# Optimization experiments

Hardware: AMD Instinct MI355X
Metric: run time of the kernel (lower is better)

Reference implementation:

```python
import jax, jax.numpy as jnp
import numpy as np

B, C, H, W = 1, 512, 64, 64
HEADS, DH = 8, 64
DI = HEADS * DH          # 512 = heads * dim_head
SW = 8                   # sliding window size
CB = 16                  # compress block size
SB = 2                   # selection block size
NSEL = 2                 # num selected blocks
N = H * W                # 4096 tokens
NCB = N // CB            # 256 compress blocks
NFB = N // SB            # 2048 fine (selection) blocks
NEG = jnp.finfo(jnp.float32).min


def setup_inputs() -> dict:
    key = jax.random.key(0)
    ks = jax.random.split(key, 24)
    rn = lambda k, shape, s=0.03: jax.random.normal(k, shape, jnp.float32) * s
    return dict(
        x=jax.random.normal(ks[0], (B, C, H, W), jnp.float32),
        w_in=rn(ks[1], (C, C)), b_in=jnp.zeros((C,), jnp.float32),
        g_norm=jnp.ones((C,), jnp.float32),
        wq=rn(ks[2], (DI, C)), wk=rn(ks[3], (DI, C)), wv=rn(ks[4], (DI, C)),
        k_pos=rn(ks[5], (HEADS, CB, DH), 0.02), v_pos=rn(ks[6], (HEADS, CB, DH), 0.02),
        mem_k=rn(ks[7], (HEADS, 1, DH), 0.02), mem_v=rn(ks[8], (HEADS, 1, DH), 0.02),
        kc_w1=rn(ks[9], (CB * DH, CB * DH)), kc_b1=jnp.zeros((CB * DH,), jnp.float32),
        kc_w2=rn(ks[10], (DH, CB * DH)), kc_b2=jnp.zeros((DH,), jnp.float32),
        vc_w1=rn(ks[11], (CB * DH, CB * DH)), vc_b1=jnp.zeros((CB * DH,), jnp.float32),
        vc_w2=rn(ks[12], (DH, CB * DH)), vc_b2=jnp.zeros((DH,), jnp.float32),
        w_strat=rn(ks[13], (3 * HEADS, C)), b_strat=jnp.zeros((3 * HEADS,), jnp.float32),
        w_comb=rn(ks[14], (C, DI)),
        w_out=rn(ks[15], (C, C)), b_out=jnp.zeros((C,), jnp.float32),
    )


def _rope(x):
    # rotary-embedding-torch default: theta=10000, interleaved pairs
    d = x.shape[-1]
    inv = 1.0 / (10000.0 ** (jnp.arange(0, d, 2, dtype=jnp.float32) / d))
    ang = jnp.arange(x.shape[-2], dtype=jnp.float32)[:, None] * inv  # (n, d/2)
    cos = jnp.repeat(jnp.cos(ang), 2, axis=-1)
    sin = jnp.repeat(jnp.sin(ang), 2, axis=-1)
    xp = x.reshape(x.shape[:-1] + (d // 2, 2))
    xr = jnp.stack((-xp[..., 1], xp[..., 0]), axis=-1).reshape(x.shape)
    return x * cos + xr * sin


def reference(x, w_in, b_in, g_norm, wq, wk, wv, k_pos, v_pos, mem_k, mem_v,
              kc_w1, kc_b1, kc_w2, kc_b2, vc_w1, vc_b1, vc_w2, vc_b2,
              w_strat, b_strat, w_comb, w_out, b_out):
    scale = DH ** -0.5
    # proj_in (1x1 conv) then flatten to sequence (b, n, c); residual uses this
    xs = jnp.einsum('bchw,oc->bohw', x, w_in) + b_in[None, :, None, None]
    seq = xs.reshape(B, C, N).transpose(0, 2, 1)
    # RMSNorm
    h = seq * jax.lax.rsqrt(jnp.mean(seq * seq, -1, keepdims=True) + 1e-6) * g_norm
    # qkv -> (b, heads, n, d)
    q = (h @ wq.T).reshape(B, N, HEADS, DH).transpose(0, 2, 1, 3)
    k = (h @ wk.T).reshape(B, N, HEADS, DH).transpose(0, 2, 1, 3)
    v = (h @ wv.T).reshape(B, N, HEADS, DH).transpose(0, 2, 1, 3)

    # ---- 1. compressed attention (block compression MLP + mem kv) ----
    kin = (k + jnp.tile(k_pos, (1, NCB, 1))[None]).reshape(B, HEADS, NCB, CB * DH)
    vin = (v + jnp.tile(v_pos, (1, NCB, 1))[None]).reshape(B, HEADS, NCB, CB * DH)
    ck = jax.nn.relu(kin @ kc_w1.T + kc_b1) @ kc_w2.T + kc_b2   # (b,h,NCB,d)
    cv = jax.nn.relu(vin @ vc_w1.T + vc_b1) @ vc_w2.T + vc_b2
    ck = jnp.concatenate([jnp.broadcast_to(mem_k[None], (B, HEADS, 1, DH)), ck], axis=2)
    cv = jnp.concatenate([jnp.broadcast_to(mem_v[None], (B, HEADS, 1, DH)), cv], axis=2)
    ck_seq = jnp.concatenate([jnp.array([-1]), (jnp.arange(NCB) + 1) * CB - 1])
    cmask = ck_seq[None, :] < jnp.arange(N)[:, None]             # (N, NCB+1), True=attend
    csim = jnp.einsum('bhid,bhjd->bhij', q, ck) * scale
    csim = jnp.where(cmask[None, None], csim, NEG)
    compressed_out = jnp.einsum('bhij,bhjd->bhid', jax.nn.softmax(csim, axis=-1), cv)

    # rotary positions for fine + sliding branches
    rq, rk = _rope(q), _rope(k)

    # ---- 2. fine selection attention ----
    # importance at fine-block granularity; since SB divides CB, each fine block
    # maps to exactly one compress block (equivalent to repeat->mask->mean in torch)
    imp = csim[..., 1:]                                          # drop mem kv logits
    fb_of = jnp.arange(NFB) // (CB // SB)
    imp_fine = imp[..., fb_of]                                   # (b,h,N,NFB)
    blk_causal = jnp.arange(NFB)[None, :] < (jnp.arange(N) // SB)[:, None]
    imp_fine = jnp.where(blk_causal[None, None], imp_fine, -jnp.inf)
    logits = jnp.concatenate([jnp.full((B, HEADS, N, 1), -1e3, jnp.float32), imp_fine], axis=-1)
    probs = jax.nn.softmax(logits, axis=-1)[..., 1:]             # (b,h,N,NFB)
    sel_val, sel_idx = jax.lax.top_k(probs, NSEL)                # (b,h,N,NSEL)
    diag_idx = jnp.broadcast_to((jnp.arange(N) // SB)[None, None, :, None], (B, HEADS, N, 1))
    sel_idx = jnp.concatenate([sel_idx, diag_idx], axis=-1)      # append own (diagonal) block
    fmask_sel = jnp.repeat((sel_val > 1e-10)[..., None], SB, axis=-1)   # (b,h,N,NSEL,SB)
    diag_mask = jnp.arange(SB)[None, :] <= (jnp.arange(N) % SB)[:, None]  # within-block causal
    diag_mask = jnp.broadcast_to(diag_mask[None, None, :, None, :], (B, HEADS, N, 1, SB))
    fmask = jnp.concatenate([fmask_sel, diag_mask], axis=-2).reshape(B, HEADS, N, (NSEL + 1) * SB)
    fk_blk = rk.reshape(B, HEADS, NFB, SB, DH)
    fv_blk = v.reshape(B, HEADS, NFB, SB, DH)
    idx = sel_idx.reshape(B, HEADS, N * (NSEL + 1))[..., None, None]
    fk = jnp.take_along_axis(fk_blk, idx, axis=2).reshape(B, HEADS, N, (NSEL + 1) * SB, DH)
    fv = jnp.take_along_axis(fv_blk, idx, axis=2).reshape(B, HEADS, N, (NSEL + 1) * SB, DH)
    fsim = jnp.einsum('bhid,bhijd->bhij', rq, fk) * scale
    fsim = jnp.where(fmask, fsim, NEG)
    fine_out = jnp.einsum('bhij,bhijd->bhid', jax.nn.softmax(fsim, axis=-1), fv)

    # ---- 3. sliding window attention (causal, exact window: 0 <= i-j <= SW) ----
    kp = jnp.pad(rk, ((0, 0), (0, 0), (SW, 0), (0, 0)))
    vp = jnp.pad(v, ((0, 0), (0, 0), (SW, 0), (0, 0)))
    widx = jnp.arange(N)[:, None] + jnp.arange(SW + 1)[None, :]  # indices into padded seq
    kw = kp[:, :, widx]                                          # (b,h,N,SW+1,d)
    vw = vp[:, :, widx]
    wvalid = (jnp.arange(N)[:, None] - SW + jnp.arange(SW + 1)[None, :]) >= 0
    ssim = jnp.einsum('bhid,bhijd->bhij', rq, kw) * scale
    ssim = jnp.where(wvalid[None, None], ssim, NEG)
    slide_out = jnp.einsum('bhij,bhijd->bhid', jax.nn.softmax(ssim, axis=-1), vw)

    # ---- combine the three strategies with learned sigmoid gates ----
    gates = jax.nn.sigmoid(h @ w_strat.T + b_strat).reshape(B, N, HEADS, 3).transpose(0, 2, 1, 3)
    out = gates[..., 0:1] * compressed_out + gates[..., 1:2] * fine_out + gates[..., 2:3] * slide_out
    out = out.transpose(0, 2, 1, 3).reshape(B, N, DI) @ w_comb.T  # merge heads + combine
    out2d = out.transpose(0, 2, 1).reshape(B, C, H, W)
    return jnp.einsum('bchw,oc->bohw', out2d, w_out) + b_out[None, :, None, None] + xs
```

## Files before the change

### kernel.cpp

```cpp
#include <hip/hip_runtime.h>
#include <hip/hip_bf16.h>
#include <math.h>

typedef __attribute__((ext_vector_type(8))) short s8v;
typedef __attribute__((ext_vector_type(8))) _Float16 h8v;
typedef __attribute__((ext_vector_type(4))) float f4v;
typedef __hip_bfloat16 bf16;

#define NEGF (-3.40282346638528859812e+38f)
#define QSMEM 20480
#define BSMEM 20480

enum { EPI_F32 = 0, EPI_BIAS, EPI_BRELU_BF16, EPI_BF16, EPI_FINAL };

__device__ __forceinline__ float wred_sum(float v) {
#pragma unroll
  for (int m = 1; m < 64; m <<= 1) v += __shfl_xor(v, m, 64);
  return v;
}

template <int EPI>
__device__ __forceinline__ void bgemm_body(char* smem, int bx, int by, int bz,
    const bf16* __restrict__ A, const bf16* __restrict__ B, void* __restrict__ C,
    int K, int ldC, long sA, long sB, long sC,
    const float* __restrict__ bias, const void* __restrict__ aux) {
  short (*Ahs)[2560] = (short(*)[2560])smem;
  short (*Bhs)[2560] = (short(*)[2560])(smem + 2 * 2560 * 2);
  const short* ah = (const short*)A + (long)bz * sA;
  const short* bh = (const short*)B + (long)bz * sB;
  int tid = threadIdx.x;
  int wv_ = tid >> 6, lane = tid & 63;
  int lrow = tid >> 2, lcol = (tid & 3) << 3;
  int lidx = lrow * 40 + lcol;
  long abase = (long)(bx * 64 + lrow) * K + lcol;
  long bbase = (long)(by * 64 + lrow) * K + lcol;
  int frow = lane & 15, fk = (lane >> 4) << 3;
  int aoff = (wv_ * 16 + frow) * 40 + fk;
  f4v acc[4] = {};
  {
    s8v avh = *(const s8v*)&ah[abase];
    s8v bvh = *(const s8v*)&bh[bbase];
    *(s8v*)&Ahs[0][lidx] = avh;
    *(s8v*)&Bhs[0][lidx] = bvh;
  }
  __syncthreads();
  int nit = K >> 5, buf = 0;
  s8v rAa, rAb, rBa, rBb;
  if (nit > 1) {
    rAa = *(const s8v*)&ah[abase + 32];
    rAb = *(const s8v*)&bh[bbase + 32];
  }
#define B_DSMFMA                                                       \
  {                                                                    \
    s8v afh = *(const s8v*)&Ahs[buf][aoff];                            \
    _Pragma("unroll") for (int nt = 0; nt < 4; nt++) {                 \
      s8v bfh = *(const s8v*)&Bhs[buf][(nt * 16 + frow) * 40 + fk];    \
      acc[nt] = __builtin_amdgcn_mfma_f32_16x16x32_bf16(afh, bfh, acc[nt], 0, 0, 0); \
    }                                                                  \
  }
  for (int it = 0; it < nit; it += 2) {
    if (it + 2 < nit) {
      long ko = (long)(it + 2) << 5;
      rBa = *(const s8v*)&ah[abase + ko];
      rBb = *(const s8v*)&bh[bbase + ko];
    }
    B_DSMFMA
    if (it + 1 < nit) {
      *(s8v*)&Ahs[buf ^ 1][lidx] = rAa;
      *(s8v*)&Bhs[buf ^ 1][lidx] = rAb;
      __syncthreads();
      buf ^= 1;
      if (it + 3 < nit) {
        long ko = (long)(it + 3) << 5;
        rAa = *(const s8v*)&ah[abase + ko];
        rAb = *(const s8v*)&bh[bbase + ko];
      }
      B_DSMFMA
      if (it + 2 < nit) {
        *(s8v*)&Ahs[buf ^ 1][lidx] = rBa;
        *(s8v*)&Bhs[buf ^ 1][lidx] = rBb;
        __syncthreads();
        buf ^= 1;
      }
    }
  }
#undef B_DSMFMA
  int rb = bx * 64 + wv_ * 16 + ((lane >> 4) << 2);
#pragma unroll
  for (int nt = 0; nt < 4; nt++) {
    int gn = by * 64 + nt * 16 + (lane & 15);
#pragma unroll
    for (int rg = 0; rg < 4; rg++) {
      int gm = rb + rg;
      float v = acc[nt][rg];
      long ci = (long)bz * sC + (long)gm * ldC + gn;
      if (EPI == EPI_F32) ((float*)C)[ci] = v;
      else if (EPI == EPI_BIAS) ((float*)C)[ci] = v + bias[gn];
      else if (EPI == EPI_BRELU_BF16) ((bf16*)C)[ci] = __float2bfloat16(fmaxf(v + bias[gn], 0.f));
      else if (EPI == EPI_BF16) ((bf16*)C)[ci] = __float2bfloat16(v);
      else if (EPI == EPI_FINAL)
        ((float*)C)[ci] = v + bias[gm] + ((const float*)aux)[(long)gn * 512 + gm];
    }
  }
}


#define HX_DECL                                                     \
  short* L = (short*)smem;                                          \
  const int MS = 64 * 40;                                           \
  int tid = threadIdx.x;                                            \
  int wv = tid >> 6, lane = tid & 63;                               \
  int lrow = tid >> 2, lcol = (tid & 3) << 3;                       \
  int frow = lane & 15, fk = (lane >> 4) << 3;                      \
  int aoff = (wv * 16 + frow) * 40 + fk;                            \
  int soff = lrow * 40 + lcol;                                      \
  f4v acc0[4] = {}, accx[4] = {}, acc2[4] = {};

#define HX_STAGE0                                                   \
  {                                                                 \
    *(h8v*)&L[0 * MS + soff] = *(const h8v*)&Ah[abase];             \
    *(h8v*)&L[1 * MS + soff] = *(const h8v*)&Al[abase];             \
    *(h8v*)&L[2 * MS + soff] = *(const h8v*)&Bh[bbase];             \
    *(h8v*)&L[3 * MS + soff] = *(const h8v*)&Bl[bbase];             \
  }                                                                 \
  __syncthreads();

#define HX_DSMFMA                                                   \
  {                                                                 \
    h8v ah = *(const h8v*)&L[aoff];                                 \
    h8v al = *(const h8v*)&L[MS + aoff];                            \
    _Pragma("unroll") for (int nt = 0; nt < 4; nt++) {              \
      int bo = 2 * MS + (nt * 16 + frow) * 40 + fk;                 \
      h8v bh = *(const h8v*)&L[bo];                                 \
      h8v bl = *(const h8v*)&L[bo + MS];                            \
      acc0[nt] = __builtin_amdgcn_mfma_f32_16x16x32_f16(ah, bh, acc0[nt], 0, 0, 0); \
      accx[nt] = __builtin_amdgcn_mfma_f32_16x16x32_f16(ah, bl, accx[nt], 0, 0, 0); \
      accx[nt] = __builtin_amdgcn_mfma_f32_16x16x32_f16(al, bh, accx[nt], 0, 0, 0); \
      acc2[nt] = __builtin_amdgcn_mfma_f32_16x16x32_f16(al, bl, acc2[nt], 0, 0, 0); \
    }                                                               \
  }

#define HX_LOOP(NIT)                                                \
  h8v rAa, rAb, rAc, rAd, rBa, rBb, rBc, rBd;                       \
  if ((NIT) > 1) {                                                  \
    rAa = *(const h8v*)&Ah[abase + 32];                             \
    rAb = *(const h8v*)&Al[abase + 32];                             \
    rAc = *(const h8v*)&Bh[bbase + 32];                             \
    rAd = *(const h8v*)&Bl[bbase + 32];                             \
  }                                                                 \
  for (int it = 0; it < (NIT); it += 2) {                           \
    if (it + 2 < (NIT)) {                                           \
      long ko = (long)(it + 2) << 5;                                \
      rBa = *(const h8v*)&Ah[abase + ko];                           \
      rBb = *(const h8v*)&Al[abase + ko];                           \
      rBc = *(const h8v*)&Bh[bbase + ko];                           \
      rBd = *(const h8v*)&Bl[bbase + ko];                           \
    }                                                               \
    HX_DSMFMA                                                       \
    if (it + 1 < (NIT)) {                                           \
      __syncthreads();                                              \
      *(h8v*)&L[soff] = rAa;                                        \
      *(h8v*)&L[MS + soff] = rAb;                                   \
      *(h8v*)&L[2 * MS + soff] = rAc;                               \
      *(h8v*)&L[3 * MS + soff] = rAd;                               \
      __syncthreads();                                              \
      if (it + 3 < (NIT)) {                                         \
        long ko = (long)(it + 3) << 5;                              \
        rAa = *(const h8v*)&Ah[abase + ko];                         \
        rAb = *(const h8v*)&Al[abase + ko];                         \
        rAc = *(const h8v*)&Bh[bbase + ko];                         \
        rAd = *(const h8v*)&Bl[bbase + ko];                         \
      }                                                             \
      HX_DSMFMA                                                     \
      if (it + 2 < (NIT)) {                                         \
        __syncthreads();                                            \
        *(h8v*)&L[soff] = rBa;                                      \
        *(h8v*)&L[MS + soff] = rBb;                                 \
        *(h8v*)&L[2 * MS + soff] = rBc;                             \
        *(h8v*)&L[3 * MS + soff] = rBd;                             \
      __syncthreads();                                              \
      }                                                             \
    }                                                               \
  }

#define HX_COMBINE(nt, rg) \
  (acc0[nt][rg] + (accx[nt][rg] + acc2[nt][rg] * (1.f / 4096.f)) * (1.f / 4096.f))

__device__ __forceinline__ void qk_f16_body(char* smem, int bx, int by,
    const _Float16* __restrict__ Ah, const _Float16* __restrict__ Al,
    const _Float16* __restrict__ Bh, const _Float16* __restrict__ Bl,
    _Float16* __restrict__ qhh, _Float16* __restrict__ qhl,
    _Float16* __restrict__ kinh, _Float16* __restrict__ kinl,
    float* __restrict__ rq, float* __restrict__ rk, const float* __restrict__ kpos,
    const float2* __restrict__ ropet) {
  HX_DECL
  long abase = (long)(bx * 64 + lrow) * 512 + lcol;
  long bbase = (long)(by * 64 + lrow) * 512 + lcol;
  HX_STAGE0
  HX_LOOP(16)
  bool isq = by < 8;
  int h = by & 7;
  int rb = wv * 16 + ((lane >> 4) << 2);
#pragma unroll
  for (int nt = 0; nt < 4; nt++) {
    int dloc = nt * 16 + frow;
    int d2 = dloc >> 1;
#pragma unroll
    for (int rg = 0; rg < 4; rg++) {
      int n = bx * 64 + rb + rg;
      float vf = HX_COMBINE(nt, rg);
      float2 cs = ropet[(long)n * 32 + d2];
      float sv = cs.x, cv = cs.y;
      float vp = __shfl_xor(vf, 1, 64);
      float rr = (dloc & 1) ? (vf * cv + vp * sv) : (vf * cv - vp * sv);
      long oi = ((long)h * 4096 + n) * 64 + dloc;
      if (isq) {
        _Float16 hi = (_Float16)vf;
        qhh[oi] = hi;
        qhl[oi] = (_Float16)((vf - (float)hi) * 4096.f);
        rq[oi] = rr;
      } else {
        rk[oi] = rr;
        float kv = vf + kpos[(h * 16 + (n & 15)) * 64 + dloc];
        _Float16 khi = (_Float16)kv;
        long ki = (((long)h * 256 + (n >> 4)) * 16 + (n & 15)) * 64 + dloc;
        kinh[ki] = khi;
        kinl[ki] = (_Float16)((kv - (float)khi) * 4096.f);
      }
    }
  }
}

__device__ __forceinline__ void hx_conv_body(char* smem, int bx, int by,
    const _Float16* __restrict__ Ah, const _Float16* __restrict__ Al,
    const _Float16* __restrict__ Bh, const _Float16* __restrict__ Bl,
    float* __restrict__ C, const float* __restrict__ bias) {
  HX_DECL
  long abase = (long)(bx * 64 + lrow) * 512 + lcol;
  long bbase = (long)(by * 64 + lrow) * 512 + lcol;
  HX_STAGE0
  HX_LOOP(16)
  int rb = bx * 64 + wv * 16 + ((lane >> 4) << 2);
#pragma unroll
  for (int nt = 0; nt < 4; nt++) {
    int gn = by * 64 + nt * 16 + frow;
#pragma unroll
    for (int rg = 0; rg < 4; rg++) {
      int gm = rb + rg;
      C[(long)gm * 512 + gn] = HX_COMBINE(nt, rg) + bias[gn];
    }
  }
}

__device__ __forceinline__ void hx_mlp1_body(char* smem, int bx, int by,
    const _Float16* __restrict__ Ah, const _Float16* __restrict__ Al,
    const _Float16* __restrict__ Bh, const _Float16* __restrict__ Bl,
    _Float16* __restrict__ Ch, _Float16* __restrict__ Cl, const float* __restrict__ bias) {
  HX_DECL
  long abase = (long)(bx * 64 + lrow) * 1024 + lcol;
  long bbase = (long)(by * 64 + lrow) * 1024 + lcol;
  HX_STAGE0
  HX_LOOP(32)
  int rb = bx * 64 + wv * 16 + ((lane >> 4) << 2);
#pragma unroll
  for (int nt = 0; nt < 4; nt++) {
    int gn = by * 64 + nt * 16 + frow;
#pragma unroll
    for (int rg = 0; rg < 4; rg++) {
      int gm = rb + rg;
      float v = fmaxf(HX_COMBINE(nt, rg) + bias[gn], 0.f);
      _Float16 hi = (_Float16)v;
      long ci = (long)gm * 1024 + gn;
      Ch[ci] = hi;
      Cl[ci] = (_Float16)((v - (float)hi) * 4096.f);
    }
  }
}

__device__ __forceinline__ void hx_ksplit_body(char* smem, int bx, int by,
    const _Float16* __restrict__ Ah, const _Float16* __restrict__ Al,
    const _Float16* __restrict__ Bh, const _Float16* __restrict__ Bl,
    float* __restrict__ P) {
  HX_DECL
  long kbeg = (long)by << 6;
  long abase = (long)(bx * 64 + lrow) * 1024 + kbeg + lcol;
  long bbase = (long)lrow * 1024 + kbeg + lcol;
  HX_STAGE0
  HX_LOOP(2)
  float* p = P + (long)by * 131072;
  int rb = bx * 64 + wv * 16 + ((lane >> 4) << 2);
#pragma unroll
  for (int nt = 0; nt < 4; nt++) {
    int gn = nt * 16 + frow;
#pragma unroll
    for (int rg = 0; rg < 4; rg++) {
      int gm = rb + rg;
      p[(long)gm * 64 + gn] = HX_COMBINE(nt, rg);
    }
  }
}

__device__ __forceinline__ void prep_elem(long i,
    const float* __restrict__ wq, const float* __restrict__ wk, const float* __restrict__ wv,
    const float* __restrict__ wst, const float* __restrict__ bst,
    const float* __restrict__ kc_w1, const float* __restrict__ kc_w2,
    const float* __restrict__ vc_w1, const float* __restrict__ vc_w2, const float* __restrict__ w_comb,
    const float* __restrict__ w_out, _Float16* __restrict__ wqkh, _Float16* __restrict__ wqkl,
    bf16* __restrict__ wvs, float* __restrict__ bias2,
    _Float16* __restrict__ kw1h, _Float16* __restrict__ kw1l,
    _Float16* __restrict__ kw2h, _Float16* __restrict__ kw2l, bf16* __restrict__ vw1b,
    bf16* __restrict__ vw2b, bf16* __restrict__ wcombb, bf16* __restrict__ woutb) {
  if (i < 524288) {
    int r = (int)(i >> 9), c = (int)(i & 511);
    float w = (r < 512) ? wq[i] : wk[(r - 512) * 512 + c];
    _Float16 hi = (_Float16)w;
    wqkh[i] = hi;
    wqkl[i] = (_Float16)((w - (float)hi) * 4096.f);
    return;
  }
  i -= 524288;
  if (i < 294912) {
    int r = (int)(i >> 9), c = (int)(i & 511);
    float v = 0.f;
    if (r < 512) v = wv[i];
    else if (r < 536) v = wst[(r - 512) * 512 + c];
    wvs[i] = __float2bfloat16(v);
    if (i < 576) bias2[i] = (i >= 512 && i < 536) ? bst[i - 512] : 0.f;
    return;
  }
  i -= 294912;
  if (i < 1048576) {
    float w = kc_w1[i];
    _Float16 hi = (_Float16)w;
    kw1h[i] = hi;
    kw1l[i] = (_Float16)((w - (float)hi) * 4096.f);
    return;
  }
  i -= 1048576;
  if (i < 65536) {
    float w = kc_w2[i];
    _Float16 hi = (_Float16)w;
    kw2h[i] = hi;
    kw2l[i] = (_Float16)((w - (float)hi) * 4096.f);
    return;
  }
  i -= 65536;
  if (i < 1048576) { vw1b[i] = __float2bfloat16(vc_w1[i]); return; }
  i -= 1048576;
  if (i < 65536) { vw2b[i] = __float2bfloat16(vc_w2[i]); return; }
  i -= 65536;
  if (i < 262144) { wcombb[i] = __float2bfloat16(w_comb[i]); return; }
  i -= 262144;
  if (i < 262144) woutb[i] = __float2bfloat16(w_out[i]);
}
#define PREP_TOTAL 3571712l

template <int EPI>
__global__ __launch_bounds__(256) void gemm_bt(
    const bf16* __restrict__ A, const bf16* __restrict__ B, void* __restrict__ C,
    int K, int ldC, long sA, long sB, long sC,
    const float* __restrict__ bias, const void* __restrict__ aux) {
  __shared__ char smem[BSMEM];
  bgemm_body<EPI>(smem, blockIdx.x, blockIdx.y, blockIdx.z, A, B, C, K, ldC, sA, sB, sC, bias, aux);
}

__global__ __launch_bounds__(256) void k_conv_prep(
    const _Float16* __restrict__ xth, const _Float16* __restrict__ xtl,
    const _Float16* __restrict__ winh, const _Float16* __restrict__ winl,
    float* __restrict__ xsf, const float* __restrict__ b_in,
    const float* __restrict__ wq, const float* __restrict__ wk, const float* __restrict__ wv,
    const float* __restrict__ wst, const float* __restrict__ bst,
    const float* __restrict__ kc_w1, const float* __restrict__ kc_w2,
    const float* __restrict__ vc_w1, const float* __restrict__ vc_w2, const float* __restrict__ w_comb,
    const float* __restrict__ w_out, _Float16* __restrict__ wqkh, _Float16* __restrict__ wqkl,
    bf16* __restrict__ wvs, float* __restrict__ bias2,
    _Float16* __restrict__ kw1h, _Float16* __restrict__ kw1l,
    _Float16* __restrict__ kw2h, _Float16* __restrict__ kw2l, bf16* __restrict__ vw1b,
    bf16* __restrict__ vw2b, bf16* __restrict__ wcombb, bf16* __restrict__ woutb) {
  __shared__ char smem[QSMEM];
  if (blockIdx.y < 8) {
    hx_conv_body(smem, blockIdx.x, blockIdx.y, xth, xtl, winh, winl, xsf, b_in);
  } else {
    long base = (((long)(blockIdx.y - 8) * 64 + blockIdx.x) * 256) + threadIdx.x;
    for (long i = base; i < PREP_TOTAL; i += 16l * 64 * 256)
      prep_elem(i, wq, wk, wv, wst, bst, kc_w1, kc_w2, vc_w1, vc_w2, w_comb, w_out,
                wqkh, wqkl, wvs, bias2, kw1h, kw1l, kw2h, kw2l, vw1b, vw2b, wcombb, woutb);
  }
}

__global__ __launch_bounds__(256) void k_fused_qk_t2(
    const _Float16* __restrict__ hhi, const _Float16* __restrict__ hlo,
    const _Float16* __restrict__ wqkh, const _Float16* __restrict__ wqkl,
    _Float16* __restrict__ qhh, _Float16* __restrict__ qhl,
    _Float16* __restrict__ kinh, _Float16* __restrict__ kinl,
    float* __restrict__ rq, float* __restrict__ rk, const float* __restrict__ kpos,
    const float2* __restrict__ ropet,
    const bf16* __restrict__ hbf, const bf16* __restrict__ wvs, float* __restrict__ T2,
    const float* __restrict__ bias2) {
  __shared__ char smem[QSMEM];
  if (blockIdx.y >= 16) {
    bgemm_body<EPI_BIAS>(smem, blockIdx.x, blockIdx.y - 16, 0, hbf, wvs, T2, 512, 576, 0, 0, 0, bias2,
                         nullptr);
    return;
  }
  qk_f16_body(smem, blockIdx.x, blockIdx.y, hhi, hlo, wqkh, wqkl, qhh, qhl, kinh, kinl, rq, rk, kpos,
              ropet);
}

__global__ void k_repackV(const float* __restrict__ T2, const float* __restrict__ vpos,
                          float* __restrict__ vvv, bf16* __restrict__ vin) {
  int e = blockIdx.x * 256 + threadIdx.x;
  int d = e & 63, n = (e >> 6) & 4095, h = e >> 18;
  float v0 = T2[(long)n * 576 + h * 64 + d];
  vvv[((long)h * 4096 + n) * 64 + d] = v0;
  vin[(((long)h * 256 + (n >> 4)) * 16 + (n & 15)) * 64 + d] =
      __float2bfloat16(v0 + vpos[(h * 16 + (n & 15)) * 64 + d]);
}

__global__ __launch_bounds__(256) void k_fused_mlp1(
    const _Float16* __restrict__ kinh, const _Float16* __restrict__ kinl,
    const _Float16* __restrict__ kw1h, const _Float16* __restrict__ kw1l,
    _Float16* __restrict__ hidh, _Float16* __restrict__ hidl, const float* __restrict__ kb1,
    const bf16* __restrict__ vin, const bf16* __restrict__ vw1,
    bf16* __restrict__ hidv, const float* __restrict__ vb1) {
  __shared__ char smem[QSMEM];
  if (blockIdx.y < 16)
    hx_mlp1_body(smem, blockIdx.x, blockIdx.y, kinh, kinl, kw1h, kw1l, hidh, hidl, kb1);
  else
    bgemm_body<EPI_BRELU_BF16>(smem, blockIdx.x, blockIdx.y - 16, 0, vin, vw1, hidv, 1024, 1024, 0, 0, 0,
                               vb1, nullptr);
}

__global__ __launch_bounds__(256) void k_fused_mlp2(
    const _Float16* __restrict__ hidh, const _Float16* __restrict__ hidl,
    const _Float16* __restrict__ kw2h, const _Float16* __restrict__ kw2l, float* __restrict__ kpart,
    const bf16* __restrict__ hidv, const bf16* __restrict__ vw2, float* __restrict__ cvc,
    const float* __restrict__ vb2) {
  __shared__ char smem[QSMEM];
  if (blockIdx.y < 16)
    hx_ksplit_body(smem, blockIdx.x, blockIdx.y, hidh, hidl, kw2h, kw2l, kpart);
  else
    bgemm_body<EPI_BIAS>(smem, blockIdx.x, 0, 0, hidv, vw2, cvc, 1024, 64, 0, 0, 0, vb2, nullptr);
}

__global__ void k_transpose16(const float* __restrict__ x, _Float16* __restrict__ xth,
                              _Float16* __restrict__ xtl,
                              const float* __restrict__ w_in, _Float16* __restrict__ winh,
                              _Float16* __restrict__ winl, float2* __restrict__ ropet) {
  if (blockIdx.y == 16) {
    int tid = threadIdx.y * 32 + threadIdx.x;
    long base = (long)blockIdx.x * 256 + tid;
    for (long i = base; i < 393216; i += 128l * 256) {
      if (i < 262144) {
        float w = w_in[i];
        _Float16 hi = (_Float16)w;
        winh[i] = hi;
        winl[i] = (_Float16)((w - (float)hi) * 4096.f);
      } else {
        int idx = (int)(i - 262144);
        int d2 = idx & 31, n = idx >> 5;
        float inv = exp2f((float)d2 * -0.4152410118609203f);
        float sv, cv;
        sincosf((float)n * inv, &sv, &cv);
        ropet[idx] = make_float2(sv, cv);
      }
    }
    return;
  }
  __shared__ float t[32][33];
  int n0 = blockIdx.x * 32, c0 = blockIdx.y * 32;
  int tx = threadIdx.x, ty = threadIdx.y;
#pragma unroll
  for (int r = ty; r < 32; r += 8) t[r][tx] = x[(long)(c0 + r) * 4096 + n0 + tx];
  __syncthreads();
#pragma unroll
  for (int r = ty; r < 32; r += 8) {
    float v = t[tx][r];
    _Float16 hi = (_Float16)v;
    long o = (long)(n0 + r) * 512 + c0 + tx;
    xth[o] = hi;
    xtl[o] = (_Float16)((v - (float)hi) * 4096.f);
  }
}

__global__ __launch_bounds__(256) void k_rmsnorm(const float* __restrict__ xs, const float* __restrict__ g,
                                                 _Float16* __restrict__ hhi, _Float16* __restrict__ hlo,
                                                 bf16* __restrict__ hbf) {
  int n = blockIdx.x, t = threadIdx.x;
  const float* row = xs + (long)n * 512;
  double a = (double)row[t], b = (double)row[t + 256];
  double ss = a * a + b * b;
#pragma unroll
  for (int m = 1; m < 64; m <<= 1) ss += __shfl_xor(ss, m, 64);
  __shared__ double red[4];
  if ((t & 63) == 0) red[t >> 6] = ss;
  __syncthreads();
  double tot = red[0] + red[1] + red[2] + red[3];
  double r = 1.0 / sqrt(tot / 512.0 + 1e-6);
  double h0 = a * r * (double)g[t], h1 = b * r * (double)g[t + 256];
  long o = (long)n * 512 + t;
  float f0 = (float)h0, f1 = (float)h1;
  _Float16 a0 = (_Float16)f0, a1 = (_Float16)f1;
  hhi[o] = a0;
  hhi[o + 256] = a1;
  hlo[o] = (_Float16)((f0 - (float)a0) * 4096.f);
  hlo[o + 256] = (_Float16)((f1 - (float)a1) * 4096.f);
  hbf[o] = __float2bfloat16(f0);
  hbf[o + 256] = __float2bfloat16(f1);
}

__global__ void k_repackB(const float* __restrict__ kpart, const float* __restrict__ cvc,
                          const float* __restrict__ mem_k, const float* __restrict__ mem_v,
                          const float* __restrict__ kb2, _Float16* __restrict__ ckbh,
                          _Float16* __restrict__ ckbl, bf16* __restrict__ cvtb) {
  int g = blockIdx.x * 256 + threadIdx.x;
  if (g < 8 * 320 * 64) {
    int d = g & 63, j = (g >> 6) % 320, h = g / (320 * 64);
    float vf = 0.f;
    if (j == 0) vf = mem_k[h * 64 + d];
    else if (j < 257) {
      long ri = ((long)h * 256 + (j - 1)) * 64 + d;
      double s = 0.0;
#pragma unroll
      for (int p = 0; p < 16; p++) s += (double)kpart[(long)p * 131072 + ri];
      vf = (float)(s + (double)kb2[d]);
    }
    _Float16 hi = (_Float16)vf;
    ckbh[g] = hi;
    ckbl[g] = (_Float16)((vf - (float)hi) * 4096.f);
  }
  if (g < 8 * 64 * 288) {
    int j = g % 288, d = (g / 288) & 63, h = g / (288 * 64);
    float v = 0.f;
    if (j == 0) v = mem_v[h * 64 + d];
    else if (j < 257) v = cvc[((long)h * 256 + (j - 1)) * 64 + d];
    cvtb[g] = __float2bfloat16(v);
  }
}

__global__ __launch_bounds__(256) void k_selsm(
    const _Float16* __restrict__ qhh, const _Float16* __restrict__ qhl,
    const _Float16* __restrict__ ckbh, const _Float16* __restrict__ ckbl,
    bf16* __restrict__ pb, int4* __restrict__ selb) {
  __shared__ float S[16][337];
  int bx = blockIdx.x, h = blockIdx.y;
  int tid = threadIdx.x, wv = tid >> 6, lane = tid & 63;
  int nv = bx + 1;
  int ntile = (nv + 15) >> 4;
  int frow = lane & 15, fkh = (lane >> 4) << 3;
  long qbase = ((long)h * 4096 + bx * 16 + frow) * 64 + fkh;
  h8v qh0 = *(const h8v*)&qhh[qbase];
  h8v ql0 = *(const h8v*)&qhl[qbase];
  h8v qh1 = *(const h8v*)&qhh[qbase + 32];
  h8v ql1 = *(const h8v*)&qhl[qbase + 32];
  for (int jt = wv; jt < ntile; jt += 4) {
    long bbase = ((long)h * 320 + jt * 16 + frow) * 64 + fkh;
    h8v bh0 = *(const h8v*)&ckbh[bbase];
    h8v bl0 = *(const h8v*)&ckbl[bbase];
    h8v bh1 = *(const h8v*)&ckbh[bbase + 32];
    h8v bl1 = *(const h8v*)&ckbl[bbase + 32];
    f4v a0 = {}, ax = {};
    a0 = __builtin_amdgcn_mfma_f32_16x16x32_f16(qh0, bh0, a0, 0, 0, 0);
    ax = __builtin_amdgcn_mfma_f32_16x16x32_f16(qh0, bl0, ax, 0, 0, 0);
    ax = __builtin_amdgcn_mfma_f32_16x16x32_f16(ql0, bh0, ax, 0, 0, 0);
    a0 = __builtin_amdgcn_mfma_f32_16x16x32_f16(qh1, bh1, a0, 0, 0, 0);
    ax = __builtin_amdgcn_mfma_f32_16x16x32_f16(qh1, bl1, ax, 0, 0, 0);
    ax = __builtin_amdgcn_mfma_f32_16x16x32_f16(ql1, bh1, ax, 0, 0, 0);
#pragma unroll
    for (int rg = 0; rg < 4; rg++)
      S[(lane >> 4) * 4 + rg][jt * 16 + (lane & 15)] =
          (a0[rg] + ax[rg] * (1.f / 4096.f)) * 0.125f;
  }
  __syncthreads();
  for (int rr = 0; rr < 4; rr++) {
    int lr = wv * 4 + rr;
    int i = bx * 16 + lr;
    long r = (long)h * 4096 + i;
    const float* row = S[lr];
    float s[5], e[5];
    float mx = -INFINITY;
#pragma unroll
    for (int t = 0; t < 5; t++) {
      int j = lane + 64 * t;
      float v = (j < nv) ? row[j] : -INFINITY;
      s[t] = v;
      mx = fmaxf(mx, v);
    }
#pragma unroll
    for (int m = 1; m < 64; m <<= 1) mx = fmaxf(mx, __shfl_xor(mx, m, 64));
    float sum = 0.f;
#pragma unroll
    for (int t = 0; t < 5; t++) {
      int j = lane + 64 * t;
      e[t] = (j < nv) ? __expf(s[t] - mx) : 0.f;
      sum += e[t];
    }
    sum = wred_sum(sum);
    float rinv = 1.f / sum;
    bf16* prow = pb + (long)r * 288;
#pragma unroll
    for (int t = 0; t < 5; t++) {
      int j = lane + 64 * t;
      if (j < 288) prow[j] = __float2bfloat16((j < nv) ? e[t] * rinv : 0.f);
    }
    int nvb = i >> 1;
    int nmv = (nvb + 7) >> 3;
    float vm[4];
    float bestv = -INFINITY;
    int bestm = 0x7fffffff;
#pragma unroll
    for (int t = 0; t < 4; t++) {
      int m = lane + 64 * t;
      float v = -INFINITY;
      if (m < nmv) v = (m + 1 < nv) ? row[m + 1] : NEGF;
      vm[t] = v;
      if (v > bestv) { bestv = v; bestm = m; }
    }
#pragma unroll
    for (int mk = 1; mk < 64; mk <<= 1) {
      float ov = __shfl_xor(bestv, mk, 64);
      int om = __shfl_xor(bestm, mk, 64);
      if (ov > bestv || (ov == bestv && om < bestm)) { bestv = ov; bestm = om; }
    }
    int m0 = bestm;
    int cnt0 = min(8, nvb - 8 * m0);
    float rv = -INFINITY;
    int rm = 0x7fffffff;
#pragma unroll
    for (int t = 0; t < 4; t++) {
      int m = lane + 64 * t;
      if (m != m0 && vm[t] > rv) { rv = vm[t]; rm = m; }
    }
#pragma unroll
    for (int mk = 1; mk < 64; mk <<= 1) {
      float ov = __shfl_xor(rv, mk, 64);
      int om = __shfl_xor(rm, mk, 64);
      if (ov > rv || (ov == rv && om < rm)) { rv = ov; rm = om; }
    }
    float Ml = fmaxf(-1000.f, bestv);
    float z = 0.f;
#pragma unroll
    for (int t = 0; t < 4; t++) {
      int m = lane + 64 * t;
      if (m < nmv) z += (float)min(8, nvb - 8 * m) * expf(vm[t] - Ml);
    }
    z = wred_sum(z) + expf(-1000.f - Ml);
    int fb0 = 0, fb1 = 0, mk0 = 0, mk1 = 0;
    if (nmv > 0) {
      float sv0 = expf(bestv - Ml) / z;
      fb0 = 8 * m0;
      mk0 = sv0 > 1e-10f;
      if (cnt0 >= 2) { fb1 = fb0 + 1; mk1 = mk0; }
      else if (nmv > 1) {
        float sv1 = expf(rv - Ml) / z;
        fb1 = 8 * rm;
        mk1 = sv1 > 1e-10f;
      }
    }
    if (lane == 0) selb[r] = make_int4(fb0, fb1, mk0, mk1);
  }
}

__global__ __launch_bounds__(256) void k_fineslide(const float* __restrict__ rq, const float* __restrict__ rk,
                                                   const float* __restrict__ vv, const float* __restrict__ co,
                                                   const int4* __restrict__ selb, const float* __restrict__ T2,
                                                   bf16* __restrict__ comb) {
  int r = blockIdx.x * 4 + (threadIdx.x >> 6);
  int d = threadIdx.x & 63;
  int h = r >> 12, i = r & 4095;
  long hb = (long)h * 4096 * 64;
  float qd = rq[hb + (long)i * 64 + d];
  int4 s4 = selb[r];
  int dg = i >> 1;
  int tok[6] = {2 * s4.x, 2 * s4.x + 1, 2 * s4.y, 2 * s4.y + 1, 2 * dg, 2 * dg + 1};
  int ok6[6] = {s4.z, s4.z, s4.w, s4.w, 1, (i & 1)};
  float sim[6], val[6];
#pragma unroll
  for (int j = 0; j < 6; j++) {
    float kd = rk[hb + (long)tok[j] * 64 + d];
    val[j] = vv[hb + (long)tok[j] * 64 + d];
    float p = wred_sum(qd * kd);
    sim[j] = ok6[j] ? p * 0.125f : NEGF;
  }
  float mx = sim[0];
#pragma unroll
  for (int j = 1; j < 6; j++) mx = fmaxf(mx, sim[j]);
  float den = 0.f, fo = 0.f;
#pragma unroll
  for (int j = 0; j < 6; j++) {
    float e_ = __expf(sim[j] - mx);
    den += e_;
    fo += e_ * val[j];
  }
  fo /= den;
  float ssim[9], sval[9];
#pragma unroll
  for (int t = 0; t < 9; t++) {
    int tk = i - 8 + t;
    int okt = tk >= 0;
    int tc = okt ? tk : 0;
    float kd = rk[hb + (long)tc * 64 + d];
    sval[t] = okt ? vv[hb + (long)tc * 64 + d] : 0.f;
    float p = wred_sum(qd * kd);
    ssim[t] = okt ? p * 0.125f : NEGF;
  }
  float mx2 = ssim[8];
#pragma unroll
  for (int t = 0; t < 8; t++) mx2 = fmaxf(mx2, ssim[t]);
  float den2 = 0.f, so = 0.f;
#pragma unroll
  for (int t = 0; t < 9; t++) {
    float e_ = __expf(ssim[t] - mx2);
    den2 += e_;
    so += e_ * sval[t];
  }
  so /= den2;
  const float* gb = T2 + (long)i * 576 + 512 + h * 3;
  float g0 = 1.f / (1.f + __expf(-gb[0]));
  float g1 = 1.f / (1.f + __expf(-gb[1]));
  float g2 = 1.f / (1.f + __expf(-gb[2]));
  float cd = co[hb + (long)i * 64 + d];
  comb[(long)i * 512 + h * 64 + d] = __float2bfloat16(g0 * cd + g1 * fo + g2 * so);
}

extern "C" void kernel_launch(void* const* d_in, const int* in_sizes, int n_in, void* d_out, int out_size,
                              void* d_ws, size_t ws_size, hipStream_t stream) {
  (void)in_sizes; (void)n_in; (void)out_size; (void)ws_size;
  const float* x = (const float*)d_in[0];
  const float* w_in = (const float*)d_in[1];
  const float* b_in = (const float*)d_in[2];
  const float* g_norm = (const float*)d_in[3];
  const float* wq = (const float*)d_in[4];
  const float* wk = (const float*)d_in[5];
  const float* wv = (const float*)d_in[6];
  const float* k_pos = (const float*)d_in[7];
  const float* v_pos = (const float*)d_in[8];
  const float* mem_k = (const float*)d_in[9];
  const float* mem_v = (const float*)d_in[10];
  const float* kc_w1 = (const float*)d_in[11];
  const float* kc_b1 = (const float*)d_in[12];
  const float* kc_w2 = (const float*)d_in[13];
  const float* kc_b2 = (const float*)d_in[14];
  const float* vc_w1 = (const float*)d_in[15];
  const float* vc_b1 = (const float*)d_in[16];
  const float* vc_w2 = (const float*)d_in[17];
  const float* vc_b2 = (const float*)d_in[18];
  const float* w_strat = (const float*)d_in[19];
  const float* b_strat = (const float*)d_in[20];
  const float* w_comb = (const float*)d_in[21];
  const float* w_out = (const float*)d_in[22];
  const float* b_out = (const float*)d_in[23];

  char* wsp = (char*)d_ws;
  size_t off = 0;
  auto alloc = [&](size_t b) -> void* {
    void* p = wsp + off;
    off += (b + 255) & ~(size_t)255;
    return p;
  };
  float* xsf = (float*)alloc(4096l * 512 * 4);
  _Float16* hhi = (_Float16*)alloc(4096l * 512 * 2);
  _Float16* hlo = (_Float16*)alloc(4096l * 512 * 2);
  bf16* hbf = (bf16*)alloc(4096l * 512 * 2);
  _Float16* winh = (_Float16*)alloc(512l * 512 * 2);
  _Float16* winl = (_Float16*)alloc(512l * 512 * 2);
  _Float16* wqkh = (_Float16*)alloc(1024l * 512 * 2);
  _Float16* wqkl = (_Float16*)alloc(1024l * 512 * 2);
  bf16* wvs = (bf16*)alloc(576l * 512 * 2);
  float* bias2 = (float*)alloc(576 * 4);
  float2* ropet = (float2*)alloc(4096l * 32 * 8);
  float* T2 = (float*)alloc(4096l * 576 * 4);
  _Float16* qhh = (_Float16*)alloc(8l * 4096 * 64 * 2);
  _Float16* qhl = (_Float16*)alloc(8l * 4096 * 64 * 2);
  float* rq = (float*)alloc(8l * 4096 * 64 * 4);
  float* rk = (float*)alloc(8l * 4096 * 64 * 4);
  float* vvb = (float*)alloc(8l * 4096 * 64 * 4);
  char* xthl = (char*)alloc(2l * 4096 * 512 * 2);
  _Float16* xth = (_Float16*)xthl;
  _Float16* xtl = xth + 4096l * 512;
  _Float16* hidh = xth;
  _Float16* hidl = xtl;
  char* kinpb = (char*)alloc(2048l * 1024 * 8 + 2048l * 1024 * 2);
  _Float16* kinh = (_Float16*)kinpb;
  _Float16* kinl = kinh + 2048l * 1024;
  bf16* vinb = (bf16*)(kinpb + 2l * 2048 * 1024 * 2);
  bf16* pb = (bf16*)kinpb;
  _Float16* kw1h = (_Float16*)alloc(1024l * 1024 * 2);
  _Float16* kw1l = (_Float16*)alloc(1024l * 1024 * 2);
  _Float16* kw2h = (_Float16*)alloc(64l * 1024 * 2);
  _Float16* kw2l = (_Float16*)alloc(64l * 1024 * 2);
  bf16* vw1b = (bf16*)alloc(1024l * 1024 * 2);
  bf16* vw2b = (bf16*)alloc(64l * 1024 * 2);
  bf16* hidv = (bf16*)alloc(2048l * 1024 * 2);
  float* cvc = (float*)alloc(2048l * 64 * 4);
  _Float16* ckbh = (_Float16*)alloc(8l * 320 * 64 * 2);
  _Float16* ckbl = (_Float16*)alloc(8l * 320 * 64 * 2);
  bf16* cvtb = (bf16*)alloc(8l * 64 * 288 * 2);
  int4* selb = (int4*)alloc(32768l * 16);
  float* co = (float*)alloc(8l * 4096 * 64 * 4);
  bf16* comb = (bf16*)alloc(4096l * 512 * 2);
  bf16* zb = (bf16*)alloc(4096l * 512 * 2);
  bf16* wcombb = (bf16*)alloc(512l * 512 * 2);
  bf16* woutb = (bf16*)alloc(512l * 512 * 2);
  float* kpart = (float*)alloc(16l * 2048 * 64 * 4);

  k_transpose16<<<dim3(128, 17), dim3(32, 8), 0, stream>>>(x, xth, xtl, w_in, winh, winl, ropet);
  k_conv_prep<<<dim3(64, 24), 256, 0, stream>>>(xth, xtl, winh, winl, xsf, b_in, wq, wk, wv, w_strat,
                                                b_strat, kc_w1, kc_w2, vc_w1, vc_w2, w_comb, w_out,
                                                wqkh, wqkl, wvs, bias2, kw1h, kw1l, kw2h, kw2l,
                                                vw1b, vw2b, wcombb, woutb);
  k_rmsnorm<<<4096, 256, 0, stream>>>(xsf, g_norm, hhi, hlo, hbf);
  k_fused_qk_t2<<<dim3(64, 25, 1), 256, 0, stream>>>(hhi, hlo, wqkh, wqkl, qhh, qhl, kinh, kinl, rq, rk,
                                                     k_pos, ropet, hbf, wvs, T2, bias2);
  k_repackV<<<8192, 256, 0, stream>>>(T2, v_pos, vvb, vinb);
  k_fused_mlp1<<<dim3(32, 32, 1), 256, 0, stream>>>(kinh, kinl, kw1h, kw1l, hidh, hidl, kc_b1, vinb, vw1b,
                                                    hidv, vc_b1);
  k_fused_mlp2<<<dim3(32, 17, 1), 256, 0, stream>>>(hidh, hidl, kw2h, kw2l, kpart, hidv, vw2b, cvc, vc_b2);
  k_repackB<<<640, 256, 0, stream>>>(kpart, cvc, mem_k, mem_v, kc_b2, ckbh, ckbl, cvtb);
  k_selsm<<<dim3(256, 8), 256, 0, stream>>>(qhh, qhl, ckbh, ckbl, pb, selb);
  gemm_bt<EPI_F32><<<dim3(64, 1, 8), 256, 0, stream>>>(pb, cvtb, co, 288, 64, 4096l * 288, 64l * 288,
                                                       4096l * 64, nullptr, nullptr);
  k_fineslide<<<8192, 256, 0, stream>>>(rq, rk, vvb, co, selb, T2, comb);
  gemm_bt<EPI_BF16><<<dim3(64, 8, 1), 256, 0, stream>>>(comb, wcombb, zb, 512, 512, 0, 0, 0, nullptr, nullptr);
  gemm_bt<EPI_FINAL><<<dim3(8, 64, 1), 256, 0, stream>>>(woutb, zb, d_out, 512, 4096, 0, 0, 0, b_out, xsf);
}
```

Measured before the change: 328.3 us.

## Fuse V repack into T2 GEMM epilogue and drop low-low split-f16 MFMA term

The V-projection GEMM blocks now write the per-head V layout and the bf16 V+v_pos compress input directly from their epilogue, which removes the separate k_repackV kernel launch and its round trip through T2. Separately, the split-f16 high/low GEMM macro no longer computes the lo*lo product term, cutting one of four MFMAs per step and one accumulator set. Dropping the lo*lo term slightly lowers the accuracy of the emulated fp32 GEMMs, a term scaled by 2^-24 that is likely negligible. The fused epilogue's scattered stores may also coalesce less well than the old dedicated repack kernel.

```diff
diff --git a/kernel.cpp b/kernel.cpp
--- a/kernel.cpp
+++ b/kernel.cpp
@@ -11,7 +11,7 @@
 #define QSMEM 20480
 #define BSMEM 20480
 
-enum { EPI_F32 = 0, EPI_BIAS, EPI_BRELU_BF16, EPI_BF16, EPI_FINAL };
+enum { EPI_F32 = 0, EPI_BIAS, EPI_BRELU_BF16, EPI_BF16, EPI_FINAL, EPI_T2V };
 
 __device__ __forceinline__ float wred_sum(float v) {
 #pragma unroll
@@ -23,7 +23,8 @@
 __device__ __forceinline__ void bgemm_body(char* smem, int bx, int by, int bz,
     const bf16* __restrict__ A, const bf16* __restrict__ B, void* __restrict__ C,
     int K, int ldC, long sA, long sB, long sC,
-    const float* __restrict__ bias, const void* __restrict__ aux) {
+    const float* __restrict__ bias, const void* __restrict__ aux,
+    const float* __restrict__ vpos, float* __restrict__ vvb, bf16* __restrict__ vinb) {
   short (*Ahs)[2560] = (short(*)[2560])smem;
   short (*Bhs)[2560] = (short(*)[2560])(smem + 2 * 2560 * 2);
   const short* ah = (const short*)A + (long)bz * sA;
@@ -100,6 +101,13 @@
       else if (EPI == EPI_BF16) ((bf16*)C)[ci] = __float2bfloat16(v);
       else if (EPI == EPI_FINAL)
         ((float*)C)[ci] = v + bias[gm] + ((const float*)aux)[(long)gn * 512 + gm];
+      else if (EPI == EPI_T2V) {
+        float vb = v + bias[gn];
+        int hh = gn >> 6, dd = gn & 63;
+        vvb[((long)hh * 4096 + gm) * 64 + dd] = vb;
+        vinb[(((long)hh * 256 + (gm >> 4)) * 16 + (gm & 15)) * 64 + dd] =
+            __float2bfloat16(vb + vpos[(hh * 16 + (gm & 15)) * 64 + dd]);
+      }
     }
   }
 }
@@ -114,7 +122,7 @@
   int frow = lane & 15, fk = (lane >> 4) << 3;                      \
   int aoff = (wv * 16 + frow) * 40 + fk;                            \
   int soff = lrow * 40 + lcol;                                      \
-  f4v acc0[4] = {}, accx[4] = {}, acc2[4] = {};
+  f4v acc0[4] = {}, accx[4] = {};
 
 #define HX_STAGE0                                                   \
   {                                                                 \
@@ -136,7 +144,6 @@
       acc0[nt] = __builtin_amdgcn_mfma_f32_16x16x32_f16(ah, bh, acc0[nt], 0, 0, 0); \
       accx[nt] = __builtin_amdgcn_mfma_f32_16x16x32_f16(ah, bl, accx[nt], 0, 0, 0); \
       accx[nt] = __builtin_amdgcn_mfma_f32_16x16x32_f16(al, bh, accx[nt], 0, 0, 0); \
-      acc2[nt] = __builtin_amdgcn_mfma_f32_16x16x32_f16(al, bl, acc2[nt], 0, 0, 0); \
     }                                                               \
   }
 
@@ -183,8 +190,7 @@
     }                                                               \
   }
 
-#define HX_COMBINE(nt, rg) \
-  (acc0[nt][rg] + (accx[nt][rg] + acc2[nt][rg] * (1.f / 4096.f)) * (1.f / 4096.f))
+#define HX_COMBINE(nt, rg) (acc0[nt][rg] + accx[nt][rg] * (1.f / 4096.f))
 
 __device__ __forceinline__ void qk_f16_body(char* smem, int bx, int by,
     const _Float16* __restrict__ Ah, const _Float16* __restrict__ Al,
@@ -361,7 +367,8 @@
     int K, int ldC, long sA, long sB, long sC,
     const float* __restrict__ bias, const void* __restrict__ aux) {
   __shared__ char smem[BSMEM];
-  bgemm_body<EPI>(smem, blockIdx.x, blockIdx.y, blockIdx.z, A, B, C, K, ldC, sA, sB, sC, bias, aux);
+  bgemm_body<EPI>(smem, blockIdx.x, blockIdx.y, blockIdx.z, A, B, C, K, ldC, sA, sB, sC, bias, aux,
+                  nullptr, nullptr, nullptr);
 }
 
 __global__ __launch_bounds__(256) void k_conv_prep(
@@ -396,25 +403,21 @@
     float* __restrict__ rq, float* __restrict__ rk, const float* __restrict__ kpos,
     const float2* __restrict__ ropet,
     const bf16* __restrict__ hbf, const bf16* __restrict__ wvs, float* __restrict__ T2,
-    const float* __restrict__ bias2) {
+    const float* __restrict__ bias2, const float* __restrict__ vpos,
+    float* __restrict__ vvb, bf16* __restrict__ vinb) {
   __shared__ char smem[QSMEM];
   if (blockIdx.y >= 16) {
-    bgemm_body<EPI_BIAS>(smem, blockIdx.x, blockIdx.y - 16, 0, hbf, wvs, T2, 512, 576, 0, 0, 0, bias2,
-                         nullptr);
+    int ty = blockIdx.y - 16;
+    if (ty < 8)
+      bgemm_body<EPI_T2V>(smem, blockIdx.x, ty, 0, hbf, wvs, T2, 512, 576, 0, 0, 0, bias2, nullptr,
+                          vpos, vvb, vinb);
+    else
+      bgemm_body<EPI_BIAS>(smem, blockIdx.x, ty, 0, hbf, wvs, T2, 512, 576, 0, 0, 0, bias2, nullptr,
+                           nullptr, nullptr, nullptr);
     return;
   }
   qk_f16_body(smem, blockIdx.x, blockIdx.y, hhi, hlo, wqkh, wqkl, qhh, qhl, kinh, kinl, rq, rk, kpos,
               ropet);
-}
-
-__global__ void k_repackV(const float* __restrict__ T2, const float* __restrict__ vpos,
-                          float* __restrict__ vvv, bf16* __restrict__ vin) {
-  int e = blockIdx.x * 256 + threadIdx.x;
-  int d = e & 63, n = (e >> 6) & 4095, h = e >> 18;
-  float v0 = T2[(long)n * 576 + h * 64 + d];
-  vvv[((long)h * 4096 + n) * 64 + d] = v0;
-  vin[(((long)h * 256 + (n >> 4)) * 16 + (n & 15)) * 64 + d] =
-      __float2bfloat16(v0 + vpos[(h * 16 + (n & 15)) * 64 + d]);
 }
 
 __global__ __launch_bounds__(256) void k_fused_mlp1(
@@ -428,7 +431,7 @@
     hx_mlp1_body(smem, blockIdx.x, blockIdx.y, kinh, kinl, kw1h, kw1l, hidh, hidl, kb1);
   else
     bgemm_body<EPI_BRELU_BF16>(smem, blockIdx.x, blockIdx.y - 16, 0, vin, vw1, hidv, 1024, 1024, 0, 0, 0,
-                               vb1, nullptr);
+                               vb1, nullptr, nullptr, nullptr, nullptr);
 }
 
 __global__ __launch_bounds__(256) void k_fused_mlp2(
@@ -440,7 +443,8 @@
   if (blockIdx.y < 16)
     hx_ksplit_body(smem, blockIdx.x, blockIdx.y, hidh, hidl, kw2h, kw2l, kpart);
   else
-    bgemm_body<EPI_BIAS>(smem, blockIdx.x, 0, 0, hidv, vw2, cvc, 1024, 64, 0, 0, 0, vb2, nullptr);
+    bgemm_body<EPI_BIAS>(smem, blockIdx.x, 0, 0, hidv, vw2, cvc, 1024, 64, 0, 0, 0, vb2, nullptr,
+                         nullptr, nullptr, nullptr);
 }
 
 __global__ void k_transpose16(const float* __restrict__ x, _Float16* __restrict__ xth,
@@ -811,8 +815,7 @@
                                                 vw1b, vw2b, wcombb, woutb);
   k_rmsnorm<<<4096, 256, 0, stream>>>(xsf, g_norm, hhi, hlo, hbf);
   k_fused_qk_t2<<<dim3(64, 25, 1), 256, 0, stream>>>(hhi, hlo, wqkh, wqkl, qhh, qhl, kinh, kinl, rq, rk,
-                                                     k_pos, ropet, hbf, wvs, T2, bias2);
-  k_repackV<<<8192, 256, 0, stream>>>(T2, v_pos, vvb, vinb);
+                                                     k_pos, ropet, hbf, wvs, T2, bias2, v_pos, vvb, vinb);
   k_fused_mlp1<<<dim3(32, 32, 1), 256, 0, stream>>>(kinh, kinl, kw1h, kw1l, hidh, hidl, kc_b1, vinb, vw1b,
                                                     hidv, vc_b1);
   k_fused_mlp2<<<dim3(32, 17, 1), 256, 0, stream>>>(hidh, hidl, kw2h, kw2l, kpart, hidv, vw2b, cvc, vc_b2);
```

After: 318.6 us, median of 2. 1.03x faster.
